# Kernel tuning notes

Hardware: AMD Instinct MI355X
Metric: run time of the kernel (lower is better)

## Reference

```python
import jax, jax.numpy as jnp
import numpy as np

EPSILON = 1e-8
PSD_EPS = 1e-5


def _mask_norm(mask):
    # torch.norm(mask, inf, dim=1, keepdim=True): max |.| over F axis
    max_abs = jnp.max(jnp.abs(mask), axis=1, keepdims=True)
    return mask / (max_abs + EPSILON)


def _estimate_psd(mask, cm):
    # mask: [B,F,T] real; cm: [B,C,F,T] complex -> psd [B,F,C,C]
    x = jnp.transpose(cm, (0, 2, 1, 3))            # [B,F,C,T]
    m = mask[:, :, None, :]                        # [B,F,1,T]
    nom = jnp.einsum('bfct,bfdt->bfcd', x * m, jnp.conj(x))
    den = jnp.clip(jnp.sum(m, axis=-1, keepdims=True), PSD_EPS, None)
    psd = nom / den
    return psd + 1j * jnp.asarray(PSD_EPS, psd.real.dtype)


def setup_inputs() -> dict:
    key = jax.random.key(0)
    k1, k2, k3, k4 = jax.random.split(key, 4)
    B, C, F, T = 8, 8, 257, 1500
    return {
        'speech_mask': jax.random.uniform(k1, (B, F, T), dtype=jnp.float32),
        'noise_mask': jax.random.uniform(k2, (B, F, T), dtype=jnp.float32),
        'cm_real': jax.random.normal(k3, (B, C, F, T), dtype=jnp.float32),
        'cm_imag': jax.random.normal(k4, (B, C, F, T), dtype=jnp.float32),
    }


def reference(speech_mask, noise_mask, cm_real, cm_imag):
    eps = EPSILON
    cm = cm_real + 1j * cm_imag                    # [B,C,F,T] complex64
    B, C, F, T = cm.shape

    sm = _mask_norm(speech_mask)
    nm = _mask_norm(noise_mask)

    speech_psd = _estimate_psd(sm, cm) + 1j * jnp.float32(eps)   # [B,F,C,C]
    noise_psd = _estimate_psd(nm, cm) + 1j * jnp.float32(eps)

    # diagonal loading + inverse, stabilized
    eye = jnp.eye(C, dtype=noise_psd.dtype)
    noise_psd_inv = jnp.linalg.inv(noise_psd + eye * eps)
    noise_psd_inv = noise_psd_inv + 1j * jnp.float32(eps)

    A = noise_psd_inv @ speech_psd                 # [B,F,C,C]
    tr = jnp.einsum('bfcc->bf', A) + eps           # trace [B,F]

    ref_vec = jnp.zeros((B, C), dtype=A.dtype).at[:, 0].set(1.0)
    u = jnp.einsum('bfcd,bd->bfc', A, ref_vec)     # [B,F,C]
    weight = u / tr[..., None]                     # [B,F,C]
    w = jnp.transpose(weight, (0, 2, 1))           # [B,C,F]

    # apply beamformer: sum_c conj(w) * cm -> [B,F,T]
    out = jnp.einsum('bcf,bcft->bft', jnp.conj(w), cm)
    return jnp.stack([out.real, out.imag])         # [2,B,F,T] float32
```

## Files before the change

kernel.cpp:

```cpp
#include <hip/hip_runtime.h>

#define Bb 8
#define Cc 8
#define Ff 257
#define Tt 1500
#define P2 750
#define BF (Bb*Ff)

__device__ __forceinline__ constexpr int utIdx(int c, int d) { return c*(17-c)/2 + (d-c); }
__device__ __forceinline__ constexpr int odIdx(int c, int d) { return 7*c - c*(c-1)/2 + (d-c-1); }

constexpr float EPSv   = 1e-8f;
constexpr float PSDEPS = 1e-5f;
constexpr float IMADD  = 1e-5f + 1e-8f;

__global__ void mask_pmax(const float* __restrict__ sm, const float* __restrict__ nm,
                          float* __restrict__ pmax_s, float* __restrict__ pmax_n) {
    int t  = blockIdx.x * 256 + threadIdx.x;
    int ch = blockIdx.y;
    int b  = blockIdx.z;
    if (t >= Tt) return;
    int f0 = ch * 33, f1 = min(Ff, f0 + 33);
    float ms = 0.f, mn = 0.f;
    for (int f = f0; f < f1; ++f) {
        ms = fmaxf(ms, fabsf(sm[(b*Ff + f)*Tt + t]));
        mn = fmaxf(mn, fabsf(nm[(b*Ff + f)*Tt + t]));
    }
    pmax_s[(b*8 + ch)*Tt + t] = ms;
    pmax_n[(b*8 + ch)*Tt + t] = mn;
}

__global__ void mask_inv(const float* __restrict__ pmax_s, const float* __restrict__ pmax_n,
                         float* __restrict__ inv_s, float* __restrict__ inv_n) {
    int t = blockIdx.x * 256 + threadIdx.x;
    int b = blockIdx.y;
    if (t >= Tt) return;
    float ms = 0.f, mn = 0.f;
    #pragma unroll
    for (int ch = 0; ch < 8; ++ch) {
        ms = fmaxf(ms, pmax_s[(b*8 + ch)*Tt + t]);
        mn = fmaxf(mn, pmax_n[(b*8 + ch)*Tt + t]);
    }
    inv_s[b*Tt + t] = 1.0f / (ms + EPSv);
    inv_n[b*Tt + t] = 1.0f / (mn + EPSv);
}

__global__ __launch_bounds__(64, 2) void mvdr_main(
    const float* __restrict__ smask, const float* __restrict__ nmask,
    const float* __restrict__ cmr,   const float* __restrict__ cmi,
    const float* __restrict__ inv_s, const float* __restrict__ inv_n,
    float* __restrict__ out)
{
    const int blk = blockIdx.x;
    const int b = blk / Ff, f = blk % Ff;
    const int tid = threadIdx.x;

    const float2* sm2 = (const float2*)smask + (b*Ff + f)*P2;
    const float2* nm2 = (const float2*)nmask + (b*Ff + f)*P2;
    const float2* is2 = (const float2*)inv_s + b*P2;
    const float2* in2 = (const float2*)inv_n + b*P2;
    const int cstride = Ff * P2;
    const float2* xr2 = (const float2*)cmr + (b*Cc)*cstride + f*P2;
    const float2* xi2 = (const float2*)cmi + (b*Cc)*cstride + f*P2;

    float accS[64], accN[64];
    #pragma unroll
    for (int v = 0; v < 64; ++v) { accS[v] = 0.f; accN[v] = 0.f; }
    float sum_ms = 0.f, sum_mn = 0.f;

    for (int p = tid; p < P2; p += 64) {
        float2 s2  = sm2[p], n2v = nm2[p];
        float2 i2s = is2[p], i2n = in2[p];
        float2 xr[8], xi[8];
        #pragma unroll
        for (int c = 0; c < 8; ++c) { xr[c] = xr2[p + c*cstride]; xi[c] = xi2[p + c*cstride]; }
        float msx = s2.x * i2s.x, msy = s2.y * i2s.y;
        float mnx = n2v.x * i2n.x, mny = n2v.y * i2n.y;
        sum_ms += msx + msy; sum_mn += mnx + mny;
        #pragma unroll
        for (int c = 0; c < 8; ++c) {
            float sax = msx*xr[c].x, say = msy*xr[c].y, sbx = msx*xi[c].x, sby = msy*xi[c].y;
            float nax = mnx*xr[c].x, nay = mny*xr[c].y, nbx = mnx*xi[c].x, nby = mny*xi[c].y;
            #pragma unroll
            for (int d = c; d < 8; ++d) {
                const int k = utIdx(c, d);
                accS[k] += sax*xr[d].x + sbx*xi[d].x + say*xr[d].y + sby*xi[d].y;
                accN[k] += nax*xr[d].x + nbx*xi[d].x + nay*xr[d].y + nby*xi[d].y;
                if (d > c) {
                    const int j = 36 + odIdx(c, d);
                    accS[j] += sbx*xr[d].x - sax*xi[d].x + sby*xr[d].y - say*xi[d].y;
                    accN[j] += nbx*xr[d].x - nax*xi[d].x + nby*xr[d].y - nay*xi[d].y;
                }
            }
        }
    }

    #pragma unroll
    for (int o = 32; o; o >>= 1) {
        sum_ms += __shfl_xor(sum_ms, o, 64);
        sum_mn += __shfl_xor(sum_mn, o, 64);
    }
    const float den_s = fmaxf(sum_ms, PSDEPS);
    const float den_n = fmaxf(sum_mn, PSDEPS);

    __shared__ float red[64*68];
    #pragma unroll
    for (int v = 0; v < 64; ++v) red[v*68 + tid] = accS[v];
    __syncthreads();
    float Sval = 0.f;
    {
        const float4* row = (const float4*)(red + tid*68);
        #pragma unroll
        for (int q = 0; q < 16; ++q) { float4 r4 = row[q]; Sval += r4.x + r4.y + r4.z + r4.w; }
    }
    __syncthreads();
    #pragma unroll
    for (int v = 0; v < 64; ++v) red[v*68 + tid] = accN[v];
    __syncthreads();
    float Nval = 0.f;
    {
        const float4* row = (const float4*)(red + tid*68);
        #pragma unroll
        for (int q = 0; q < 16; ++q) { float4 r4 = row[q]; Nval += r4.x + r4.y + r4.z + r4.w; }
    }

    __shared__ float SreM[64], SimM[64];
    __shared__ float Are[128], Aim[128];
    __shared__ float dre[8], dim_[8], wre[8], wim[8];

    {
        int cc_, dd_;
        if (tid < 36) { int k = tid, c = 0; while (k >= 8 - c) { k -= 8 - c; ++c; } cc_ = c; dd_ = c + k; }
        else          { int k = tid - 36, c = 0; while (k >= 7 - c) { k -= 7 - c; ++c; } cc_ = c; dd_ = c + k + 1; }
        float sv = Sval / den_s, nv = Nval / den_n;
        if (tid < 36) {
            SreM[cc_*8 + dd_] = sv; SreM[dd_*8 + cc_] = sv;
            float nvd = nv + (cc_ == dd_ ? EPSv : 0.f);
            Are[cc_*16 + dd_] = nvd; Are[dd_*16 + cc_] = nvd;
            if (cc_ == dd_) { SimM[cc_*8 + cc_] = IMADD; Aim[cc_*16 + cc_] = IMADD; }
        } else {
            SimM[cc_*8 + dd_] = IMADD + sv; SimM[dd_*8 + cc_] = IMADD - sv;
            Aim[cc_*16 + dd_] = IMADD + nv; Aim[dd_*16 + cc_] = IMADD - nv;
        }
        int r = tid >> 3, j = tid & 7;
        Are[r*16 + 8 + j] = (r == j) ? 1.f : 0.f;
        Aim[r*16 + 8 + j] = 0.f;
    }
    __syncthreads();

    {
        const int r = tid >> 3, cA = tid & 7;
        for (int k = 0; k < 8; ++k) {
            float pr = Are[k*16 + k], pi = Aim[k*16 + k];
            float idn = 1.0f / (pr*pr + pi*pi);
            float ipr = pr*idn, ipi = -pi*idn;
            if (r == k) {
                float ar0 = Are[k*16 + cA],     ai0 = Aim[k*16 + cA];
                Are[k*16 + cA]     = ar0*ipr - ai0*ipi; Aim[k*16 + cA]     = ar0*ipi + ai0*ipr;
                float ar1 = Are[k*16 + cA + 8], ai1 = Aim[k*16 + cA + 8];
                Are[k*16 + cA + 8] = ar1*ipr - ai1*ipi; Aim[k*16 + cA + 8] = ar1*ipi + ai1*ipr;
            }
            __syncthreads();
            float fr = Are[r*16 + k], fi = Aim[r*16 + k];
            float p0r = Are[k*16 + cA],     p0i = Aim[k*16 + cA];
            float p1r = Are[k*16 + cA + 8], p1i = Aim[k*16 + cA + 8];
            float o0r = 0.f, o0i = 0.f, o1r = 0.f, o1i = 0.f;
            if (r != k) {
                o0r = Are[r*16 + cA]     - (fr*p0r - fi*p0i);
                o0i = Aim[r*16 + cA]     - (fr*p0i + fi*p0r);
                o1r = Are[r*16 + cA + 8] - (fr*p1r - fi*p1i);
                o1i = Aim[r*16 + cA + 8] - (fr*p1i + fi*p1r);
            }
            __syncthreads();
            if (r != k) {
                Are[r*16 + cA]     = o0r; Aim[r*16 + cA]     = o0i;
                Are[r*16 + cA + 8] = o1r; Aim[r*16 + cA + 8] = o1i;
            }
            __syncthreads();
        }
    }

    if (tid < 8) {
        int c = tid;
        float ur = 0.f, ui = 0.f, tr_r = 0.f, tr_i = 0.f;
        #pragma unroll
        for (int j = 0; j < 8; ++j) {
            float vr = Are[c*16 + 8 + j], vi = Aim[c*16 + 8 + j] + EPSv;
            float s0r = SreM[j*8 + 0], s0i = SimM[j*8 + 0];
            ur += vr*s0r - vi*s0i; ui += vr*s0i + vi*s0r;
            float scr = SreM[j*8 + c], sci = SimM[j*8 + c];
            tr_r += vr*scr - vi*sci; tr_i += vr*sci + vi*scr;
        }
        dre[c] = tr_r; dim_[c] = tr_i;
        wre[c] = ur;   wim[c]  = ui;
    }
    __syncthreads();
    if (tid < 8) {
        float tr_r = EPSv, tr_i = 0.f;
        #pragma unroll
        for (int j = 0; j < 8; ++j) { tr_r += dre[j]; tr_i += dim_[j]; }
        float idn = 1.0f / (tr_r*tr_r + tr_i*tr_i);
        float ur = wre[tid], ui = wim[tid];
        wre[tid] = (ur*tr_r + ui*tr_i) * idn;
        wim[tid] = (ui*tr_r - ur*tr_i) * idn;
    }
    __syncthreads();

    float wr[8], wi[8];
    #pragma unroll
    for (int c = 0; c < 8; ++c) { wr[c] = wre[c]; wi[c] = wim[c]; }

    float2* outr = (float2*)out + (b*Ff + f)*P2;
    float2* outi = (float2*)out + (Bb*Ff)*P2 + (b*Ff + f)*P2;
    for (int p = tid; p < P2; p += 64) {
        float rx = 0.f, ry = 0.f, ix = 0.f, iy = 0.f;
        #pragma unroll
        for (int c = 0; c < 8; ++c) {
            float2 a  = xr2[p + c*cstride];
            float2 bb = xi2[p + c*cstride];
            rx += wr[c]*a.x + wi[c]*bb.x;
            ry += wr[c]*a.y + wi[c]*bb.y;
            ix += wr[c]*bb.x - wi[c]*a.x;
            iy += wr[c]*bb.y - wi[c]*a.y;
        }
        outr[p] = make_float2(rx, ry);
        outi[p] = make_float2(ix, iy);
    }
}

extern "C" void kernel_launch(void* const* d_in, const int* in_sizes, int n_in,
                              void* d_out, int out_size, void* d_ws, size_t ws_size,
                              hipStream_t stream) {
    const float* smask = (const float*)d_in[0];
    const float* nmask = (const float*)d_in[1];
    const float* cmr   = (const float*)d_in[2];
    const float* cmi   = (const float*)d_in[3];
    float* ws = (float*)d_ws;
    float* pmax_s = ws;
    float* pmax_n = ws + 96000;
    float* inv_s  = ws + 192000;
    float* inv_n  = ws + 204000;

    mask_pmax<<<dim3(6, 8, 8), 256, 0, stream>>>(smask, nmask, pmax_s, pmax_n);
    mask_inv <<<dim3(6, 8),    256, 0, stream>>>(pmax_s, pmax_n, inv_s, inv_n);
    mvdr_main<<<BF, 64, 0, stream>>>(smask, nmask, cmr, cmi, inv_s, inv_n, (float*)d_out);
}
```

Measured before the change: 312.1 us.

## Split speech/noise PSD accumulation across thread pairs with 256-thread blocks

Each block now runs 256 threads instead of 64. Adjacent thread pairs share the same time samples, with one thread accumulating the speech PSD and the other the noise PSD, so each thread keeps 64 accumulators instead of 128. This lowers register pressure and raises occupancy and memory-level parallelism on a bandwidth-bound kernel. In exchange, each pair loads the channel data twice and pays for an extra shuffle plus shared-memory reduction stage, and the inversion step runs only 64 active lanes.

```diff
diff --git a/kernel.cpp b/kernel.cpp
--- a/kernel.cpp
+++ b/kernel.cpp
@@ -45,7 +45,7 @@
     inv_n[b*Tt + t] = 1.0f / (mn + EPSv);
 }
 
-__global__ __launch_bounds__(64, 2) void mvdr_main(
+__global__ __launch_bounds__(256, 3) void mvdr_main(
     const float* __restrict__ smask, const float* __restrict__ nmask,
     const float* __restrict__ cmr,   const float* __restrict__ cmi,
     const float* __restrict__ inv_s, const float* __restrict__ inv_n,
@@ -53,82 +53,106 @@
 {
     const int blk = blockIdx.x;
     const int b = blk / Ff, f = blk % Ff;
-    const int tid = threadIdx.x;
+    const int tid  = threadIdx.x;
+    const int par  = tid & 1;
+    const int pair = tid >> 1;
+    const int wid  = tid >> 6;
+    const int lane = tid & 63;
 
     const float2* sm2 = (const float2*)smask + (b*Ff + f)*P2;
     const float2* nm2 = (const float2*)nmask + (b*Ff + f)*P2;
     const float2* is2 = (const float2*)inv_s + b*P2;
     const float2* in2 = (const float2*)inv_n + b*P2;
+    const float2* m2  = par ? nm2 : sm2;
+    const float2* iv2 = par ? in2 : is2;
     const int cstride = Ff * P2;
     const float2* xr2 = (const float2*)cmr + (b*Cc)*cstride + f*P2;
     const float2* xi2 = (const float2*)cmi + (b*Cc)*cstride + f*P2;
 
-    float accS[64], accN[64];
-    #pragma unroll
-    for (int v = 0; v < 64; ++v) { accS[v] = 0.f; accN[v] = 0.f; }
-    float sum_ms = 0.f, sum_mn = 0.f;
-
-    for (int p = tid; p < P2; p += 64) {
-        float2 s2  = sm2[p], n2v = nm2[p];
-        float2 i2s = is2[p], i2n = in2[p];
-        float2 xr[8], xi[8];
-        #pragma unroll
-        for (int c = 0; c < 8; ++c) { xr[c] = xr2[p + c*cstride]; xi[c] = xi2[p + c*cstride]; }
-        float msx = s2.x * i2s.x, msy = s2.y * i2s.y;
-        float mnx = n2v.x * i2n.x, mny = n2v.y * i2n.y;
-        sum_ms += msx + msy; sum_mn += mnx + mny;
-        #pragma unroll
-        for (int c = 0; c < 8; ++c) {
-            float sax = msx*xr[c].x, say = msy*xr[c].y, sbx = msx*xi[c].x, sby = msy*xi[c].y;
-            float nax = mnx*xr[c].x, nay = mny*xr[c].y, nbx = mnx*xi[c].x, nby = mny*xi[c].y;
+    float acc[64];
+    #pragma unroll
+    for (int v = 0; v < 64; ++v) acc[v] = 0.f;
+    float summ = 0.f;
+
+    int p = pair;
+    #pragma unroll 1
+    for (int it = 0; it < 6; ++it, p += 128) {
+        if (p < P2) {
+            float2 mk = m2[p], iv = iv2[p];
+            float2 xr[8], xi[8];
             #pragma unroll
-            for (int d = c; d < 8; ++d) {
-                const int k = utIdx(c, d);
-                accS[k] += sax*xr[d].x + sbx*xi[d].x + say*xr[d].y + sby*xi[d].y;
-                accN[k] += nax*xr[d].x + nbx*xi[d].x + nay*xr[d].y + nby*xi[d].y;
-                if (d > c) {
+            for (int c = 0; c < 8; ++c) { xr[c] = xr2[p + c*cstride]; xi[c] = xi2[p + c*cstride]; }
+            float mx = mk.x * iv.x, my = mk.y * iv.y;
+            summ += mx + my;
+            #pragma unroll
+            for (int c = 0; c < 8; ++c) {
+                float ax = mx*xr[c].x, ay = my*xr[c].y, bx = mx*xi[c].x, by = my*xi[c].y;
+                {
+                    const int k = utIdx(c, c);
+                    float t0 = acc[k];
+                    t0 = fmaf(ax, xr[c].x, t0); t0 = fmaf(bx, xi[c].x, t0);
+                    t0 = fmaf(ay, xr[c].y, t0); t0 = fmaf(by, xi[c].y, t0);
+                    acc[k] = t0;
+                }
+                #pragma unroll
+                for (int d = c + 1; d < 8; ++d) {
+                    const int k = utIdx(c, d);
                     const int j = 36 + odIdx(c, d);
-                    accS[j] += sbx*xr[d].x - sax*xi[d].x + sby*xr[d].y - say*xi[d].y;
-                    accN[j] += nbx*xr[d].x - nax*xi[d].x + nby*xr[d].y - nay*xi[d].y;
+                    float t0 = acc[k], t1 = acc[j];
+                    t0 = fmaf(ax, xr[d].x, t0); t0 = fmaf(bx, xi[d].x, t0);
+                    t0 = fmaf(ay, xr[d].y, t0); t0 = fmaf(by, xi[d].y, t0);
+                    t1 = fmaf(bx, xr[d].x, t1); t1 = fmaf(-ax, xi[d].x, t1);
+                    t1 = fmaf(by, xr[d].y, t1); t1 = fmaf(-ay, xi[d].y, t1);
+                    acc[k] = t0; acc[j] = t1;
                 }
             }
         }
     }
 
     #pragma unroll
-    for (int o = 32; o; o >>= 1) {
-        sum_ms += __shfl_xor(sum_ms, o, 64);
-        sum_mn += __shfl_xor(sum_mn, o, 64);
-    }
-    const float den_s = fmaxf(sum_ms, PSDEPS);
-    const float den_n = fmaxf(sum_mn, PSDEPS);
-
-    __shared__ float red[64*68];
-    #pragma unroll
-    for (int v = 0; v < 64; ++v) red[v*68 + tid] = accS[v];
+    for (int o = 2; o <= 32; o <<= 1) summ += __shfl_xor(summ, o, 64);
+    __shared__ float msum[4], nsum[4];
+    if (lane == 0) msum[wid] = summ;
+    if (lane == 1) nsum[wid] = summ;
+
+    #pragma unroll
+    for (int v = 0; v < 64; ++v) {
+        acc[v] += __shfl_xor(acc[v], 2, 64);
+        acc[v] += __shfl_xor(acc[v], 4, 64);
+    }
+    __shared__ float red[64*36];
+    const int col = wid*8 + (lane >> 3);
+    if (par == 0 && (lane & 7) == 0) {
+        #pragma unroll
+        for (int v = 0; v < 64; ++v) red[v*36 + col] = acc[v];
+    }
     __syncthreads();
     float Sval = 0.f;
-    {
-        const float4* row = (const float4*)(red + tid*68);
-        #pragma unroll
-        for (int q = 0; q < 16; ++q) { float4 r4 = row[q]; Sval += r4.x + r4.y + r4.z + r4.w; }
-    }
-    __syncthreads();
-    #pragma unroll
-    for (int v = 0; v < 64; ++v) red[v*68 + tid] = accN[v];
+    if (tid < 64) {
+        const float4* row = (const float4*)(red + tid*36);
+        #pragma unroll
+        for (int k = 0; k < 8; ++k) { float4 r4 = row[k]; Sval += r4.x + r4.y + r4.z + r4.w; }
+    }
+    __syncthreads();
+    if (par == 1 && (lane & 7) == 1) {
+        #pragma unroll
+        for (int v = 0; v < 64; ++v) red[v*36 + col] = acc[v];
+    }
     __syncthreads();
     float Nval = 0.f;
-    {
-        const float4* row = (const float4*)(red + tid*68);
-        #pragma unroll
-        for (int q = 0; q < 16; ++q) { float4 r4 = row[q]; Nval += r4.x + r4.y + r4.z + r4.w; }
+    if (tid < 64) {
+        const float4* row = (const float4*)(red + tid*36);
+        #pragma unroll
+        for (int k = 0; k < 8; ++k) { float4 r4 = row[k]; Nval += r4.x + r4.y + r4.z + r4.w; }
     }
 
     __shared__ float SreM[64], SimM[64];
     __shared__ float Are[128], Aim[128];
     __shared__ float dre[8], dim_[8], wre[8], wim[8];
 
-    {
+    if (tid < 64) {
+        const float den_s = fmaxf(msum[0]+msum[1]+msum[2]+msum[3], PSDEPS);
+        const float den_n = fmaxf(nsum[0]+nsum[1]+nsum[2]+nsum[3], PSDEPS);
         int cc_, dd_;
         if (tid < 36) { int k = tid, c = 0; while (k >= 8 - c) { k -= 8 - c; ++c; } cc_ = c; dd_ = c + k; }
         else          { int k = tid - 36, c = 0; while (k >= 7 - c) { k -= 7 - c; ++c; } cc_ = c; dd_ = c + k + 1; }
@@ -149,12 +173,13 @@
     __syncthreads();
 
     {
-        const int r = tid >> 3, cA = tid & 7;
+        const bool act = tid < 64;
+        const int r = (tid >> 3) & 7, cA = tid & 7;
         for (int k = 0; k < 8; ++k) {
             float pr = Are[k*16 + k], pi = Aim[k*16 + k];
             float idn = 1.0f / (pr*pr + pi*pi);
             float ipr = pr*idn, ipi = -pi*idn;
-            if (r == k) {
+            if (act && r == k) {
                 float ar0 = Are[k*16 + cA],     ai0 = Aim[k*16 + cA];
                 Are[k*16 + cA]     = ar0*ipr - ai0*ipi; Aim[k*16 + cA]     = ar0*ipi + ai0*ipr;
                 float ar1 = Are[k*16 + cA + 8], ai1 = Aim[k*16 + cA + 8];
@@ -172,7 +197,7 @@
                 o1i = Aim[r*16 + cA + 8] - (fr*p1i + fi*p1r);
             }
             __syncthreads();
-            if (r != k) {
+            if (act && r != k) {
                 Are[r*16 + cA]     = o0r; Aim[r*16 + cA]     = o0i;
                 Are[r*16 + cA + 8] = o1r; Aim[r*16 + cA + 8] = o1i;
             }
@@ -212,19 +237,19 @@
 
     float2* outr = (float2*)out + (b*Ff + f)*P2;
     float2* outi = (float2*)out + (Bb*Ff)*P2 + (b*Ff + f)*P2;
-    for (int p = tid; p < P2; p += 64) {
+    for (int pp = tid; pp < P2; pp += 256) {
         float rx = 0.f, ry = 0.f, ix = 0.f, iy = 0.f;
         #pragma unroll
         for (int c = 0; c < 8; ++c) {
-            float2 a  = xr2[p + c*cstride];
-            float2 bb = xi2[p + c*cstride];
+            float2 a  = xr2[pp + c*cstride];
+            float2 bb = xi2[pp + c*cstride];
             rx += wr[c]*a.x + wi[c]*bb.x;
             ry += wr[c]*a.y + wi[c]*bb.y;
             ix += wr[c]*bb.x - wi[c]*a.x;
             iy += wr[c]*bb.y - wi[c]*a.y;
         }
-        outr[p] = make_float2(rx, ry);
-        outi[p] = make_float2(ix, iy);
+        outr[pp] = make_float2(rx, ry);
+        outi[pp] = make_float2(ix, iy);
     }
 }
 
@@ -243,5 +268,5 @@
 
     mask_pmax<<<dim3(6, 8, 8), 256, 0, stream>>>(smask, nmask, pmax_s, pmax_n);
     mask_inv <<<dim3(6, 8),    256, 0, stream>>>(pmax_s, pmax_n, inv_s, inv_n);
-    mvdr_main<<<BF, 64, 0, stream>>>(smask, nmask, cmr, cmi, inv_s, inv_n, (float*)d_out);
-}
+    mvdr_main<<<BF, 256, 0, stream>>>(smask, nmask, cmr, cmi, inv_s, inv_n, (float*)d_out);
+}
```

Result: faster. 301.4 us (-3.5%).
